# Optimization experiments

Measured on AMD Instinct MI355X. Metric: run time of the kernel, lower is better.

The kernel has to match this reference:

```python
import jax, jax.numpy as jnp
import numpy as np

N, E, IN, OUT, MC, H, C, HID = 50000, 800000, 64, 64, 16, 4, 16, 128
NEG = 0.2   # leaky_relu negative slope
EPS = 1e-5  # BatchNorm eps


def _gcn(x, src, dst, norm, W, b):
    # GCNConv: symmetric-normalized aggregation with self-loops already in (src, dst)
    h = x @ W
    return jax.ops.segment_sum(h[src] * norm[:, None], dst, num_segments=N) + b


def _gat(x, src, dst, W, b, a_s, a_d):
    # GATConv, concat=True: h -> [N, H, C]
    h = (x @ W).reshape(N, H, C)
    e = jax.nn.leaky_relu((h * a_s).sum(-1)[src] + (h * a_d).sum(-1)[dst], NEG)  # [E+N, H]
    m = jax.ops.segment_max(e, dst, num_segments=N)
    p = jnp.exp(e - m[dst])
    alpha = p / jax.ops.segment_sum(p, dst, num_segments=N)[dst]
    out = jax.ops.segment_sum(h[src] * alpha[..., None], dst, num_segments=N)
    return out.reshape(N, H * C) + b


def _bn(x):
    # BatchNorm(affine=False), training stats (biased variance)
    mu = x.mean(0)
    var = x.var(0)
    return (x - mu) / jnp.sqrt(var + EPS)


def _spade(x, mask, src, dst, norm, w0, b0, wg, bg, wb, bb):
    mf = jax.nn.relu(_gcn(mask, src, dst, norm, w0, b0))
    gamma = _gcn(mf, src, dst, norm, wg, bg)
    beta = _gcn(mf, src, dst, norm, wb, bb)
    return _bn(x) * (1.0 + gamma) + beta


def _forward(x, mask, edge_index, params):
    s1, s2, sk, g1, g2, gk = params
    loop = jnp.arange(N, dtype=edge_index.dtype)  # self-loops (GCN & GAT defaults)
    src = jnp.concatenate([edge_index[0], loop])
    dst = jnp.concatenate([edge_index[1], loop])
    deg = jax.ops.segment_sum(jnp.ones(src.shape[0], x.dtype), dst, num_segments=N)
    dinv = jnp.where(deg > 0, jax.lax.rsqrt(deg), 0.0)
    norm = dinv[src] * dinv[dst]
    xm = jax.nn.leaky_relu(_spade(x, mask, src, dst, norm, *s1), NEG)
    xm = _gat(xm, src, dst, *g1)
    xm = jax.nn.leaky_relu(_spade(xm, mask, src, dst, norm, *s2), NEG)
    xm = _gat(xm, src, dst, *g2)
    xs = jax.nn.leaky_relu(_spade(x, mask, src, dst, norm, *sk), NEG)
    xs = _gat(xs, src, dst, *gk)
    return xm + xs


def setup_inputs() -> dict:
    key = jax.random.key(0)
    ks = iter(jax.random.split(key, 40))
    def rn(shape, scale=1.0):
        return jax.random.normal(next(ks), shape, jnp.float32) * scale
    inp = {
        "x": rn((N, IN)),
        "mask": rn((N, MC)),
        "edge_index": jax.random.randint(next(ks), (2, E), 0, N, dtype=jnp.int32),
    }
    for p in ("s1", "s2", "sk"):
        inp[p + "_w0"] = rn((MC, HID), 0.1)
        inp[p + "_b0"] = jnp.zeros(HID, jnp.float32)
        inp[p + "_wg"] = rn((HID, IN), 0.05)
        inp[p + "_bg"] = jnp.zeros(IN, jnp.float32)
        inp[p + "_wb"] = rn((HID, IN), 0.05)
        inp[p + "_bb"] = jnp.zeros(IN, jnp.float32)
    for g, din in (("g1", IN), ("g2", OUT), ("gk", IN)):
        inp[g + "_w"] = rn((din, H * C), 0.1)
        inp[g + "_b"] = jnp.zeros(H * C, jnp.float32)
        inp[g + "_as"] = rn((H, C), 0.1)
        inp[g + "_ad"] = rn((H, C), 0.1)
    return inp


def reference(x, mask, edge_index,
              s1_w0, s1_b0, s1_wg, s1_bg, s1_wb, s1_bb,
              s2_w0, s2_b0, s2_wg, s2_bg, s2_wb, s2_bb,
              sk_w0, sk_b0, sk_wg, sk_bg, sk_wb, sk_bb,
              g1_w, g1_b, g1_as, g1_ad,
              g2_w, g2_b, g2_as, g2_ad,
              gk_w, gk_b, gk_as, gk_ad):
    params = (
        (s1_w0, s1_b0, s1_wg, s1_bg, s1_wb, s1_bb),
        (s2_w0, s2_b0, s2_wg, s2_bg, s2_wb, s2_bb),
        (sk_w0, sk_b0, sk_wg, sk_bg, sk_wb, sk_bb),
        (g1_w, g1_b, g1_as, g1_ad),
        (g2_w, g2_b, g2_as, g2_ad),
        (gk_w, gk_b, gk_as, gk_ad),
    )
    return _forward(x, mask, edge_index, params)
```

## Files before the change

### kernel.cpp

```cpp
#include <hip/hip_runtime.h>
#include <hip/hip_bf16.h>

constexpr int kN   = 50000;
constexpr int kE   = 800000;
constexpr int kIN  = 64;
constexpr int kMC  = 16;
constexpr int kH   = 4;
constexpr int kC   = 16;
constexpr int kHID = 128;
constexpr float kNEG = 0.2f;
constexpr float kEPS = 1e-5f;

__device__ __forceinline__ float lrelu(float x) { return x > 0.f ? x : kNEG * x; }


__global__ void k_count(const int* __restrict__ ei, int* __restrict__ cnt) {
    int e = blockIdx.x * blockDim.x + threadIdx.x;
    if (e < kE) atomicAdd(&cnt[ei[kE + e]], 1);
}

__global__ void k_scan(const int* __restrict__ cnt, int* __restrict__ rp,
                       float* __restrict__ dinv) {
    __shared__ int wsum[16];
    __shared__ int chunk_base;
    int tid = threadIdx.x, lane = tid & 63, wid = tid >> 6;
    if (tid == 0) chunk_base = 0;
    __syncthreads();
    for (int base = 0; base < kN; base += 1024) {
        int i = base + tid;
        int v = (i < kN) ? cnt[i] : 0;
        if (i < kN) dinv[i] = rsqrtf((float)(v + 1));
        int s = v;
        #pragma unroll
        for (int off = 1; off < 64; off <<= 1) {
            int t = __shfl_up(s, off);
            if (lane >= off) s += t;
        }
        if (lane == 63) wsum[wid] = s;
        __syncthreads();
        if (wid == 0) {
            int t = (lane < 16) ? wsum[lane] : 0;
            #pragma unroll
            for (int off = 1; off < 16; off <<= 1) {
                int u = __shfl_up(t, off);
                if (lane >= off) t += u;
            }
            if (lane < 16) wsum[lane] = t;
        }
        __syncthreads();
        int wbase = (wid > 0) ? wsum[wid - 1] : 0;
        int total = wsum[15];
        int excl = chunk_base + wbase + s - v;
        if (i < kN) rp[i] = excl;
        __syncthreads();
        if (tid == 0) chunk_base += total;
        __syncthreads();
    }
    if (threadIdx.x == 0) rp[kN] = chunk_base;
}

__global__ void k_fill(const int* __restrict__ ei, const int* __restrict__ rp,
                       int* __restrict__ fill, int* __restrict__ col) {
    int e = blockIdx.x * blockDim.x + threadIdx.x;
    if (e < kE) {
        int d = ei[kE + e];
        int pos = rp[d] + atomicAdd(&fill[d], 1);
        col[pos] = ei[e];
    }
}


template <int F>
__global__ void k_agg(const float* __restrict__ in, float* __restrict__ out,
                      const float* __restrict__ dinv, const int* __restrict__ rp,
                      const int* __restrict__ col) {
    constexpr int NPB = 256 / F;
    int node = blockIdx.x * NPB + threadIdx.x / F;
    int f = threadIdx.x % F;
    if (node >= kN) return;
    float dv = dinv[node];
    float acc = dv * in[(size_t)node * F + f];
    int b = rp[node], e2 = rp[node + 1];
    for (int i = b; i < e2; ++i) {
        int u = col[i];
        acc += dinv[u] * in[(size_t)u * F + f];
    }
    out[(size_t)node * F + f] = dv * acc;
}


__global__ void k_agg128v(const float* __restrict__ in, float* __restrict__ out,
                          const float* __restrict__ dinv, const int* __restrict__ rp,
                          const int* __restrict__ col) {
    int node = blockIdx.x * 8 + threadIdx.x / 32;
    int l = threadIdx.x & 31;
    if (node >= kN) return;
    const float4* in4 = (const float4*)in;
    float dv = dinv[node];
    float4 acc = in4[(size_t)node * 32 + l];
    int b = rp[node], e2 = rp[node + 1];
    for (int base = b; base < e2; base += 32) {
        int idx = base + l;
        int myu = (idx < e2) ? col[idx] : 0;
        int n = min(32, e2 - base);
        for (int cc = 0; cc < n; ++cc) {
            int u = __shfl(myu, cc, 32);
            float4 w = in4[(size_t)u * 32 + l];
            acc.x += w.x; acc.y += w.y; acc.z += w.z; acc.w += w.w;
        }
    }
    ((float4*)out)[(size_t)node * 32 + l] =
        make_float4(dv * acc.x, dv * acc.y, dv * acc.z, dv * acc.w);
}


__global__ void k_mf(const float* __restrict__ am, const float* __restrict__ w0,
                     const float* __restrict__ b0, const float* __restrict__ dinv,
                     float* __restrict__ mf) {
    __shared__ float w[16 * 128];
    __shared__ float a[16 * 16];
    int tid = threadIdx.x;
    int n0 = blockIdx.x * 16;
    {
        const float4* w04 = (const float4*)w0;
        float4* w4 = (float4*)w;
        #pragma unroll
        for (int i = 0; i < 2; ++i) w4[tid + 256 * i] = w04[tid + 256 * i];
        if (tid < 64) {
            const float4* am4 = (const float4*)am;
            int node = n0 + tid / 4;
            ((float4*)a)[tid] = (node < kN) ? am4[(size_t)node * 4 + (tid & 3)]
                                            : make_float4(0.f, 0.f, 0.f, 0.f);
        }
    }
    __syncthreads();
    int f = tid % 128, g = tid / 128;
    float bf = b0[f];
    for (int j = 0; j < 8; ++j) {
        int nl = g * 8 + j;
        int node = n0 + nl;
        if (node < kN) {
            float acc = bf;
            #pragma unroll
            for (int k = 0; k < 16; ++k) acc += a[nl * 16 + k] * w[k * 128 + f];
            mf[(size_t)node * 128 + f] = dinv[node] * fmaxf(acc, 0.f);
        }
    }
}


__global__ void k_bnstats(const float* __restrict__ x, float* __restrict__ stats) {
    int f = threadIdx.x % 64, r0 = threadIdx.x / 64;
    float s = 0.f, s2 = 0.f;
    for (int v = blockIdx.x * 4 + r0; v < kN; v += gridDim.x * 4) {
        float val = x[(size_t)v * 64 + f];
        s += val; s2 += val * val;
    }
    __shared__ float sh[256], sh2[256];
    sh[threadIdx.x] = s; sh2[threadIdx.x] = s2;
    __syncthreads();
    if (threadIdx.x < 64) {
        s  = sh[threadIdx.x]  + sh[threadIdx.x + 64]  + sh[threadIdx.x + 128]  + sh[threadIdx.x + 192];
        s2 = sh2[threadIdx.x] + sh2[threadIdx.x + 64] + sh2[threadIdx.x + 128] + sh2[threadIdx.x + 192];
        atomicAdd(&stats[f], s);
        atomicAdd(&stats[64 + f], s2);
    }
}

__global__ void k_bnfin(const float* __restrict__ stats, float* __restrict__ mu_rstd) {
    int f = threadIdx.x;
    if (f < 64) {
        float mu = stats[f] / (float)kN;
        float var = stats[64 + f] / (float)kN - mu * mu;
        mu_rstd[f] = mu;
        mu_rstd[64 + f] = rsqrtf(var + kEPS);
    }
}


__global__ void k_spgat(const float* __restrict__ xin, const float* __restrict__ amf,
                        const float* __restrict__ wg, const float* __restrict__ bg,
                        const float* __restrict__ wb, const float* __restrict__ bb,
                        const float* __restrict__ mu_rstd,
                        const float* __restrict__ W, const float* __restrict__ as_,
                        const float* __restrict__ ad_,
                        float* __restrict__ h, float* __restrict__ esed) {
    __shared__ float smem[6144];
    float* a   = smem;
    float* wgs = smem + 2048;
    float* wbs = smem + 4096;
    float* ys  = smem;
    float* ws  = smem + 1024;
    int tid = threadIdx.x;
    int n0 = blockIdx.x * 16;
    {
        const float4* amf4 = (const float4*)amf;
        float4* a4 = (float4*)a;
        #pragma unroll
        for (int i = 0; i < 2; ++i) {
            int idx = tid + 256 * i;
            int node = n0 + idx / 32;
            a4[idx] = (node < kN) ? amf4[(size_t)node * 32 + (idx & 31)]
                                  : make_float4(0.f, 0.f, 0.f, 0.f);
        }
    }
    int f = tid % 64, nl = tid / 64;
    float accg[4] = {0, 0, 0, 0}, accb[4] = {0, 0, 0, 0};
    const float4* wg4 = (const float4*)wg;
    const float4* wb4 = (const float4*)wb;
    for (int c = 0; c < 4; ++c) {
        __syncthreads();
        {
            float4* wgs4 = (float4*)wgs;
            float4* wbs4 = (float4*)wbs;
            #pragma unroll
            for (int i = 0; i < 2; ++i) {
                int idx = tid + 256 * i;
                wgs4[idx] = wg4[c * 512 + idx];
                wbs4[idx] = wb4[c * 512 + idx];
            }
        }
        __syncthreads();
        #pragma unroll
        for (int kk = 0; kk < 32; ++kk) {
            float wgk = wgs[kk * 64 + f], wbk = wbs[kk * 64 + f];
            int k = c * 32 + kk;
            #pragma unroll
            for (int j = 0; j < 4; ++j) {
                float av = a[(j * 4 + nl) * 128 + k];
                accg[j] += av * wgk;
                accb[j] += av * wbk;
            }
        }
    }
    float mu = mu_rstd[f], rstd = mu_rstd[64 + f];
    float bgf = bg[f], bbf = bb[f];
    float yv[4];
    #pragma unroll
    for (int j = 0; j < 4; ++j) {
        int node = n0 + j * 4 + nl;
        if (node < kN) {
            float xv = xin[(size_t)node * 64 + f];
            float g = accg[j] + bgf, b = accb[j] + bbf;
            yv[j] = lrelu((xv - mu) * rstd * (1.f + g) + b);
        } else yv[j] = 0.f;
    }
    __syncthreads();
    #pragma unroll
    for (int j = 0; j < 4; ++j) ys[(j * 4 + nl) * 64 + f] = yv[j];
    {
        const float4* W4 = (const float4*)W;
        float4* ws4 = (float4*)ws;
        #pragma unroll
        for (int i = 0; i < 4; ++i) ws4[tid + 256 * i] = W4[tid + 256 * i];
    }
    __syncthreads();
    float asf = as_[f], adf = ad_[f];
    float acc[4] = {0, 0, 0, 0};
    for (int k = 0; k < 64; ++k) {
        float w = ws[k * 64 + f];
        #pragma unroll
        for (int j = 0; j < 4; ++j) acc[j] += ys[(j * 4 + nl) * 64 + k] * w;
    }
    #pragma unroll
    for (int j = 0; j < 4; ++j) {
        int node = n0 + j * 4 + nl;
        float hv = acc[j];
        float es = hv * asf, ed = hv * adf;
        #pragma unroll
        for (int off = 1; off < 16; off <<= 1) {
            es += __shfl_xor(es, off);
            ed += __shfl_xor(ed, off);
        }
        if (node < kN) {
            h[(size_t)node * 64 + f] = hv;
            if ((f & 15) == 0) {
                int hh = f >> 4;
                esed[node * 8 + hh] = es;
                esed[node * 8 + 4 + hh] = ed;
            }
        }
    }
}


__global__ void k_gatagg(const float* __restrict__ h, const float* __restrict__ esed,
                         const int* __restrict__ rp, const int* __restrict__ col,
                         const float* __restrict__ bias, float* __restrict__ out) {
    int node = blockIdx.x * 4 + threadIdx.x / 64;
    if (node >= kN) return;
    int lane = threadIdx.x & 63;
    int hh = lane >> 4;
    float edv = esed[node * 8 + 4 + hh];
    float m = lrelu(esed[node * 8 + hh] + edv);
    float d = 1.f;
    float acc = h[(size_t)node * 64 + lane];
    int b = rp[node], e2 = rp[node + 1];
    for (int base = b; base < e2; base += 64) {
        int idx = base + lane;
        int myu = (idx < e2) ? col[idx] : 0;
        int n = min(64, e2 - base);
        for (int cc = 0; cc < n; ++cc) {
            int u = __shfl(myu, cc);
            float e = lrelu(esed[u * 8 + hh] + edv);
            float hu = h[(size_t)u * 64 + lane];
            if (e <= m) {
                float p = __expf(e - m);
                d += p;
                acc += p * hu;
            } else {
                float s = __expf(m - e);
                d = d * s + 1.f;
                acc = acc * s + hu;
                m = e;
            }
        }
    }
    out[(size_t)node * 64 + lane] = acc / d + bias[lane];
}


__global__ void k_add(const float4* __restrict__ a, const float4* __restrict__ b,
                      float4* __restrict__ o, int n4) {
    int i = blockIdx.x * blockDim.x + threadIdx.x;
    if (i < n4) {
        float4 x = a[i], y = b[i];
        o[i] = make_float4(x.x + y.x, x.y + y.y, x.z + y.z, x.w + y.w);
    }
}


extern "C" void kernel_launch(void* const* d_in, const int* in_sizes, int n_in,
                              void* d_out, int out_size, void* d_ws, size_t ws_size,
                              hipStream_t stream) {
    const float* x    = (const float*)d_in[0];
    const float* mask = (const float*)d_in[1];
    const int*   ei   = (const int*)d_in[2];
    const float* s_w0[3] = {(const float*)d_in[3],  (const float*)d_in[9],  (const float*)d_in[15]};
    const float* s_b0[3] = {(const float*)d_in[4],  (const float*)d_in[10], (const float*)d_in[16]};
    const float* s_wg[3] = {(const float*)d_in[5],  (const float*)d_in[11], (const float*)d_in[17]};
    const float* s_bg[3] = {(const float*)d_in[6],  (const float*)d_in[12], (const float*)d_in[18]};
    const float* s_wb[3] = {(const float*)d_in[7],  (const float*)d_in[13], (const float*)d_in[19]};
    const float* s_bb[3] = {(const float*)d_in[8],  (const float*)d_in[14], (const float*)d_in[20]};
    const float* g_w[3]  = {(const float*)d_in[21], (const float*)d_in[25], (const float*)d_in[29]};
    const float* g_b[3]  = {(const float*)d_in[22], (const float*)d_in[26], (const float*)d_in[30]};
    const float* g_as[3] = {(const float*)d_in[23], (const float*)d_in[27], (const float*)d_in[31]};
    const float* g_ad[3] = {(const float*)d_in[24], (const float*)d_in[28], (const float*)d_in[32]};

    char* base = (char*)d_ws;
    size_t off = 0;
    auto alloc = [&](size_t bytes) -> void* {
        void* p = base + off;
        off = (off + bytes + 255) & ~(size_t)255;
        return p;
    };
    int*   cnt   = (int*)alloc((size_t)kN * 4);
    int*   rp    = (int*)alloc((size_t)(kN + 1) * 4);
    int*   fill  = (int*)alloc((size_t)kN * 4);
    int*   col   = (int*)alloc((size_t)kE * 4);
    float* dinv  = (float*)alloc((size_t)kN * 4);
    float* am    = (float*)alloc((size_t)kN * 16 * 4);
    float* P     = (float*)alloc((size_t)kN * 128 * 4);
    float* Q     = (float*)alloc((size_t)kN * 128 * 4);
    float* tH    = (float*)alloc((size_t)kN * 64 * 4);
    float* tZ    = (float*)alloc((size_t)kN * 64 * 4);
    float* tZ2   = (float*)alloc((size_t)kN * 64 * 4);
    float* esed  = (float*)alloc((size_t)kN * 8 * 4);
    float* sraw  = (float*)alloc(128 * 4);
    float* st_x  = (float*)alloc(128 * 4);
    float* st_z  = (float*)alloc(128 * 4);
    (void)ws_size; (void)n_in; (void)in_sizes; (void)out_size;

    const int EB = (kE + 255) / 256;

    hipMemsetAsync(cnt, 0, (size_t)kN * 4, stream);
    hipMemsetAsync(fill, 0, (size_t)kN * 4, stream);
    k_count<<<EB, 256, 0, stream>>>(ei, cnt);
    k_scan<<<1, 1024, 0, stream>>>(cnt, rp, dinv);
    k_fill<<<EB, 256, 0, stream>>>(ei, rp, fill, col);

    k_agg<16><<<(kN + 15) / 16, 256, 0, stream>>>(mask, am, dinv, rp, col);
    hipMemsetAsync(sraw, 0, 128 * 4, stream);
    k_bnstats<<<256, 256, 0, stream>>>(x, sraw);
    k_bnfin<<<1, 64, 0, stream>>>(sraw, st_x);

    const int GB16 = (kN + 15) / 16;
    const int GB8  = (kN + 7) / 8;
    const int GB4  = (kN + 3) / 4;

    k_mf<<<GB16, 256, 0, stream>>>(am, s_w0[0], s_b0[0], dinv, P);
    k_agg128v<<<GB8, 256, 0, stream>>>(P, Q, dinv, rp, col);
    k_spgat<<<GB16, 256, 0, stream>>>(x, Q, s_wg[0], s_bg[0], s_wb[0], s_bb[0], st_x,
                                      g_w[0], g_as[0], g_ad[0], tH, esed);
    k_gatagg<<<GB4, 256, 0, stream>>>(tH, esed, rp, col, g_b[0], tZ);

    hipMemsetAsync(sraw, 0, 128 * 4, stream);
    k_bnstats<<<256, 256, 0, stream>>>(tZ, sraw);
    k_bnfin<<<1, 64, 0, stream>>>(sraw, st_z);
    k_mf<<<GB16, 256, 0, stream>>>(am, s_w0[1], s_b0[1], dinv, P);
    k_agg128v<<<GB8, 256, 0, stream>>>(P, Q, dinv, rp, col);
    k_spgat<<<GB16, 256, 0, stream>>>(tZ, Q, s_wg[1], s_bg[1], s_wb[1], s_bb[1], st_z,
                                      g_w[1], g_as[1], g_ad[1], tH, esed);
    k_gatagg<<<GB4, 256, 0, stream>>>(tH, esed, rp, col, g_b[1], tZ2);

    k_mf<<<GB16, 256, 0, stream>>>(am, s_w0[2], s_b0[2], dinv, P);
    k_agg128v<<<GB8, 256, 0, stream>>>(P, Q, dinv, rp, col);
    k_spgat<<<GB16, 256, 0, stream>>>(x, Q, s_wg[2], s_bg[2], s_wb[2], s_bb[2], st_x,
                                      g_w[2], g_as[2], g_ad[2], tH, esed);
    k_gatagg<<<GB4, 256, 0, stream>>>(tH, esed, rp, col, g_b[2], tZ);

    k_add<<<(kN * 64 / 4 + 255) / 256, 256, 0, stream>>>((const float4*)tZ2, (const float4*)tZ,
                                                         (float4*)d_out, kN * 64 / 4);
}
```

Baseline: 1.489 ms.

## Store intermediates in fp16, batch independent branches, fuse GAT aggregations and BN prep

Intermediate mask-feature buffers and GAT hidden features are now stored as fp16, cutting gather bandwidth in the edge aggregations. The skip branch (sk/gk) is batched with the second main-path layer in shared launches, and the two final GAT aggregations are fused with the output add. BN stats finalisation is folded into the spgat kernel, the mask aggregation is merged with the x BN stats into one launch, and the memsets are consolidated. Bounds checks are removed on the assumption that N divides by 16. Half precision lowers accuracy.

```diff
diff --git a/kernel.cpp b/kernel.cpp
--- a/kernel.cpp
+++ b/kernel.cpp
@@ -1,17 +1,19 @@
 #include <hip/hip_runtime.h>
-#include <hip/hip_bf16.h>
+#include <hip/hip_fp16.h>
 
 constexpr int kN   = 50000;
 constexpr int kE   = 800000;
-constexpr int kIN  = 64;
-constexpr int kMC  = 16;
-constexpr int kH   = 4;
-constexpr int kC   = 16;
-constexpr int kHID = 128;
 constexpr float kNEG = 0.2f;
 constexpr float kEPS = 1e-5f;
+constexpr int kNB16 = kN / 16;
 
 __device__ __forceinline__ float lrelu(float x) { return x > 0.f ? x : kNEG * x; }
+
+__device__ __forceinline__ void unpack8(int4 raw, float* t) {
+    __half2* h = (__half2*)&raw;
+    #pragma unroll
+    for (int i = 0; i < 4; ++i) { float2 f = __half22float2(h[i]); t[2*i] = f.x; t[2*i+1] = f.y; }
+}
 
 
 __global__ void k_count(const int* __restrict__ ei, int* __restrict__ cnt) {
@@ -70,80 +72,37 @@
 }
 
 
-template <int F>
-__global__ void k_agg(const float* __restrict__ in, float* __restrict__ out,
-                      const float* __restrict__ dinv, const int* __restrict__ rp,
-                      const int* __restrict__ col) {
-    constexpr int NPB = 256 / F;
-    int node = blockIdx.x * NPB + threadIdx.x / F;
-    int f = threadIdx.x % F;
-    if (node >= kN) return;
-    float dv = dinv[node];
-    float acc = dv * in[(size_t)node * F + f];
-    int b = rp[node], e2 = rp[node + 1];
-    for (int i = b; i < e2; ++i) {
-        int u = col[i];
-        acc += dinv[u] * in[(size_t)u * F + f];
-    }
-    out[(size_t)node * F + f] = dv * acc;
-}
-
-
-__global__ void k_agg128v(const float* __restrict__ in, float* __restrict__ out,
-                          const float* __restrict__ dinv, const int* __restrict__ rp,
-                          const int* __restrict__ col) {
-    int node = blockIdx.x * 8 + threadIdx.x / 32;
-    int l = threadIdx.x & 31;
-    if (node >= kN) return;
-    const float4* in4 = (const float4*)in;
-    float dv = dinv[node];
-    float4 acc = in4[(size_t)node * 32 + l];
-    int b = rp[node], e2 = rp[node + 1];
-    for (int base = b; base < e2; base += 32) {
-        int idx = base + l;
-        int myu = (idx < e2) ? col[idx] : 0;
-        int n = min(32, e2 - base);
-        for (int cc = 0; cc < n; ++cc) {
-            int u = __shfl(myu, cc, 32);
-            float4 w = in4[(size_t)u * 32 + l];
-            acc.x += w.x; acc.y += w.y; acc.z += w.z; acc.w += w.w;
-        }
-    }
-    ((float4*)out)[(size_t)node * 32 + l] =
-        make_float4(dv * acc.x, dv * acc.y, dv * acc.z, dv * acc.w);
-}
-
-
-__global__ void k_mf(const float* __restrict__ am, const float* __restrict__ w0,
-                     const float* __restrict__ b0, const float* __restrict__ dinv,
-                     float* __restrict__ mf) {
-    __shared__ float w[16 * 128];
-    __shared__ float a[16 * 16];
-    int tid = threadIdx.x;
-    int n0 = blockIdx.x * 16;
-    {
-        const float4* w04 = (const float4*)w0;
-        float4* w4 = (float4*)w;
-        #pragma unroll
-        for (int i = 0; i < 2; ++i) w4[tid + 256 * i] = w04[tid + 256 * i];
-        if (tid < 64) {
-            const float4* am4 = (const float4*)am;
-            int node = n0 + tid / 4;
-            ((float4*)a)[tid] = (node < kN) ? am4[(size_t)node * 4 + (tid & 3)]
-                                            : make_float4(0.f, 0.f, 0.f, 0.f);
-        }
-    }
-    __syncthreads();
-    int f = tid % 128, g = tid / 128;
-    float bf = b0[f];
-    for (int j = 0; j < 8; ++j) {
-        int nl = g * 8 + j;
-        int node = n0 + nl;
-        if (node < kN) {
-            float acc = bf;
-            #pragma unroll
-            for (int k = 0; k < 16; ++k) acc += a[nl * 16 + k] * w[k * 128 + f];
-            mf[(size_t)node * 128 + f] = dinv[node] * fmaxf(acc, 0.f);
+__global__ void k_combo(const float* __restrict__ mask, const float* __restrict__ x,
+                        const float* __restrict__ dinv, const int* __restrict__ rp,
+                        const int* __restrict__ col,
+                        float* __restrict__ am, float* __restrict__ sraw_x) {
+    if (blockIdx.x < kNB16) {
+        int node = blockIdx.x * 16 + threadIdx.x / 16;
+        int f = threadIdx.x % 16;
+        float dv = dinv[node];
+        float acc = dv * mask[(size_t)node * 16 + f];
+        int b = rp[node], e2 = rp[node + 1];
+        for (int i = b; i < e2; ++i) {
+            int u = col[i];
+            acc += dinv[u] * mask[(size_t)u * 16 + f];
+        }
+        am[(size_t)node * 16 + f] = dv * acc;
+    } else {
+        int bb = blockIdx.x - kNB16;
+        int f = threadIdx.x % 64, r0 = threadIdx.x / 64;
+        float s = 0.f, s2 = 0.f;
+        for (int v = bb * 4 + r0; v < kN; v += 256 * 4) {
+            float val = x[(size_t)v * 64 + f];
+            s += val; s2 += val * val;
+        }
+        __shared__ float sh[256], sh2[256];
+        sh[threadIdx.x] = s; sh2[threadIdx.x] = s2;
+        __syncthreads();
+        if (threadIdx.x < 64) {
+            s  = sh[threadIdx.x]  + sh[threadIdx.x + 64]  + sh[threadIdx.x + 128]  + sh[threadIdx.x + 192];
+            s2 = sh2[threadIdx.x] + sh2[threadIdx.x + 64] + sh2[threadIdx.x + 128] + sh2[threadIdx.x + 192];
+            atomicAdd(&sraw_x[f], s);
+            atomicAdd(&sraw_x[64 + f], s2);
         }
     }
 }
@@ -167,24 +126,89 @@
     }
 }
 
-__global__ void k_bnfin(const float* __restrict__ stats, float* __restrict__ mu_rstd) {
-    int f = threadIdx.x;
-    if (f < 64) {
-        float mu = stats[f] / (float)kN;
-        float var = stats[64 + f] / (float)kN - mu * mu;
-        mu_rstd[f] = mu;
-        mu_rstd[64 + f] = rsqrtf(var + kEPS);
-    }
-}
-
-
-__global__ void k_spgat(const float* __restrict__ xin, const float* __restrict__ amf,
-                        const float* __restrict__ wg, const float* __restrict__ bg,
-                        const float* __restrict__ wb, const float* __restrict__ bb,
-                        const float* __restrict__ mu_rstd,
-                        const float* __restrict__ W, const float* __restrict__ as_,
-                        const float* __restrict__ ad_,
-                        float* __restrict__ h, float* __restrict__ esed) {
+
+__global__ void k_mf2(const float* __restrict__ am,
+                      const float* __restrict__ w0a, const float* __restrict__ b0a,
+                      const float* __restrict__ w0b, const float* __restrict__ b0b,
+                      const float* __restrict__ dinv,
+                      __half* __restrict__ Pa, __half* __restrict__ Pb) {
+    int set = blockIdx.x / kNB16;
+    int blk = blockIdx.x - set * kNB16;
+    const float* w0 = set ? w0b : w0a;
+    const float* b0 = set ? b0b : b0a;
+    __half* P = set ? Pb : Pa;
+    __shared__ float w[16 * 128];
+    __shared__ float a[16 * 16];
+    int tid = threadIdx.x;
+    int n0 = blk * 16;
+    {
+        const float4* w04 = (const float4*)w0;
+        float4* w4 = (float4*)w;
+        #pragma unroll
+        for (int i = 0; i < 2; ++i) w4[tid + 256 * i] = w04[tid + 256 * i];
+        if (tid < 64) {
+            const float4* am4 = (const float4*)am;
+            int node = n0 + tid / 4;
+            ((float4*)a)[tid] = am4[(size_t)node * 4 + (tid & 3)];
+        }
+    }
+    __syncthreads();
+    int f = tid % 128, g = tid / 128;
+    float bf = b0[f];
+    for (int j = 0; j < 8; ++j) {
+        int nl = g * 8 + j;
+        int node = n0 + nl;
+        float acc = bf;
+        #pragma unroll
+        for (int k = 0; k < 16; ++k) acc += a[nl * 16 + k] * w[k * 128 + f];
+        P[(size_t)node * 128 + f] = __float2half(dinv[node] * fmaxf(acc, 0.f));
+    }
+}
+
+
+__global__ void k_aggh(const __half* __restrict__ Pa, const __half* __restrict__ Pb,
+                       __half* __restrict__ Qa, __half* __restrict__ Qb,
+                       const float* __restrict__ dinv, const int* __restrict__ rp,
+                       const int* __restrict__ col) {
+    int set = blockIdx.x / kNB16;
+    int blk = blockIdx.x - set * kNB16;
+    const int4* in = (const int4*)(set ? Pb : Pa);
+    int4* out = (int4*)(set ? Qb : Qa);
+    int node = blk * 16 + threadIdx.x / 16;
+    int l = threadIdx.x & 15;
+    float dv = dinv[node];
+    float acc[8];
+    unpack8(in[(size_t)node * 16 + l], acc);
+    int b = rp[node], e2 = rp[node + 1];
+    for (int base = b; base < e2; base += 16) {
+        int idx = base + l;
+        int myu = (idx < e2) ? col[idx] : 0;
+        int n = min(16, e2 - base);
+        for (int cc = 0; cc < n; ++cc) {
+            int u = __shfl(myu, cc, 16);
+            float t[8];
+            unpack8(in[(size_t)u * 16 + l], t);
+            #pragma unroll
+            for (int q = 0; q < 8; ++q) acc[q] += t[q];
+        }
+    }
+    int4 r;
+    __half2* hp = (__half2*)&r;
+    #pragma unroll
+    for (int i = 0; i < 4; ++i) hp[i] = __floats2half2_rn(dv * acc[2*i], dv * acc[2*i+1]);
+    out[(size_t)node * 16 + l] = r;
+}
+
+
+struct SpgatArgs {
+    const float* xin; const __half* Q;
+    const float *wg, *bg, *wb, *bb, *sraw, *W, *as_, *ad_;
+    __half* h; float* esed; int eslot;
+};
+
+__global__ void k_spgat(SpgatArgs A, SpgatArgs B) {
+    SpgatArgs P = (blockIdx.x < kNB16) ? A : B;
+    int blk = (blockIdx.x < kNB16) ? blockIdx.x : blockIdx.x - kNB16;
     __shared__ float smem[6144];
     float* a   = smem;
     float* wgs = smem + 2048;
@@ -192,22 +216,20 @@
     float* ys  = smem;
     float* ws  = smem + 1024;
     int tid = threadIdx.x;
-    int n0 = blockIdx.x * 16;
-    {
-        const float4* amf4 = (const float4*)amf;
-        float4* a4 = (float4*)a;
-        #pragma unroll
-        for (int i = 0; i < 2; ++i) {
-            int idx = tid + 256 * i;
-            int node = n0 + idx / 32;
-            a4[idx] = (node < kN) ? amf4[(size_t)node * 32 + (idx & 31)]
-                                  : make_float4(0.f, 0.f, 0.f, 0.f);
-        }
+    int n0 = blk * 16;
+    {
+        const int4* q4 = (const int4*)P.Q;
+        int node = n0 + tid / 16, h8 = tid & 15;
+        float t[8];
+        unpack8(q4[(size_t)node * 16 + h8], t);
+        float* dst = a + (tid / 16) * 128 + h8 * 8;
+        ((float4*)dst)[0] = make_float4(t[0], t[1], t[2], t[3]);
+        ((float4*)dst)[1] = make_float4(t[4], t[5], t[6], t[7]);
     }
     int f = tid % 64, nl = tid / 64;
-    float accg[4] = {0, 0, 0, 0}, accb[4] = {0, 0, 0, 0};
-    const float4* wg4 = (const float4*)wg;
-    const float4* wb4 = (const float4*)wb;
+    float accg[4] = {0,0,0,0}, accb[4] = {0,0,0,0};
+    const float4* wg4 = (const float4*)P.wg;
+    const float4* wb4 = (const float4*)P.wb;
     for (int c = 0; c < 4; ++c) {
         __syncthreads();
         {
@@ -233,30 +255,33 @@
             }
         }
     }
-    float mu = mu_rstd[f], rstd = mu_rstd[64 + f];
-    float bgf = bg[f], bbf = bb[f];
+    float mu, rstd;
+    {
+        float s = P.sraw[f], s2 = P.sraw[64 + f];
+        mu = s * (1.f / kN);
+        rstd = rsqrtf(s2 * (1.f / kN) - mu * mu + kEPS);
+    }
+    float bgf = P.bg[f], bbf = P.bb[f];
     float yv[4];
     #pragma unroll
     for (int j = 0; j < 4; ++j) {
         int node = n0 + j * 4 + nl;
-        if (node < kN) {
-            float xv = xin[(size_t)node * 64 + f];
-            float g = accg[j] + bgf, b = accb[j] + bbf;
-            yv[j] = lrelu((xv - mu) * rstd * (1.f + g) + b);
-        } else yv[j] = 0.f;
+        float xv = P.xin[(size_t)node * 64 + f];
+        float g = accg[j] + bgf, b = accb[j] + bbf;
+        yv[j] = lrelu((xv - mu) * rstd * (1.f + g) + b);
     }
     __syncthreads();
     #pragma unroll
     for (int j = 0; j < 4; ++j) ys[(j * 4 + nl) * 64 + f] = yv[j];
     {
-        const float4* W4 = (const float4*)W;
+        const float4* W4 = (const float4*)P.W;
         float4* ws4 = (float4*)ws;
         #pragma unroll
         for (int i = 0; i < 4; ++i) ws4[tid + 256 * i] = W4[tid + 256 * i];
     }
     __syncthreads();
-    float asf = as_[f], adf = ad_[f];
-    float acc[4] = {0, 0, 0, 0};
+    float asf = P.as_[f], adf = P.ad_[f];
+    float acc[4] = {0,0,0,0};
     for (int k = 0; k < 64; ++k) {
         float w = ws[k * 64 + f];
         #pragma unroll
@@ -272,29 +297,26 @@
             es += __shfl_xor(es, off);
             ed += __shfl_xor(ed, off);
         }
-        if (node < kN) {
-            h[(size_t)node * 64 + f] = hv;
-            if ((f & 15) == 0) {
-                int hh = f >> 4;
-                esed[node * 8 + hh] = es;
-                esed[node * 8 + 4 + hh] = ed;
-            }
-        }
-    }
-}
-
-
-__global__ void k_gatagg(const float* __restrict__ h, const float* __restrict__ esed,
-                         const int* __restrict__ rp, const int* __restrict__ col,
-                         const float* __restrict__ bias, float* __restrict__ out) {
+        P.h[(size_t)node * 64 + f] = __float2half(hv);
+        if ((f & 15) == 0) {
+            int hh = f >> 4;
+            P.esed[node * 16 + P.eslot + hh] = es;
+            P.esed[node * 16 + P.eslot + 4 + hh] = ed;
+        }
+    }
+}
+
+
+__global__ void k_gatagg1(const __half* __restrict__ h, const float* __restrict__ esed,
+                          const int* __restrict__ rp, const int* __restrict__ col,
+                          const float* __restrict__ bias, float* __restrict__ out) {
     int node = blockIdx.x * 4 + threadIdx.x / 64;
-    if (node >= kN) return;
     int lane = threadIdx.x & 63;
     int hh = lane >> 4;
-    float edv = esed[node * 8 + 4 + hh];
-    float m = lrelu(esed[node * 8 + hh] + edv);
+    float edv = esed[node * 16 + 4 + hh];
+    float m = lrelu(esed[node * 16 + hh] + edv);
     float d = 1.f;
-    float acc = h[(size_t)node * 64 + lane];
+    float acc = __half2float(h[(size_t)node * 64 + lane]);
     int b = rp[node], e2 = rp[node + 1];
     for (int base = b; base < e2; base += 64) {
         int idx = base + lane;
@@ -302,17 +324,14 @@
         int n = min(64, e2 - base);
         for (int cc = 0; cc < n; ++cc) {
             int u = __shfl(myu, cc);
-            float e = lrelu(esed[u * 8 + hh] + edv);
-            float hu = h[(size_t)u * 64 + lane];
+            float e = lrelu(esed[u * 16 + hh] + edv);
+            float hu = __half2float(h[(size_t)u * 64 + lane]);
             if (e <= m) {
                 float p = __expf(e - m);
-                d += p;
-                acc += p * hu;
+                d += p; acc += p * hu;
             } else {
                 float s = __expf(m - e);
-                d = d * s + 1.f;
-                acc = acc * s + hu;
-                m = e;
+                d = d * s + 1.f; acc = acc * s + hu; m = e;
             }
         }
     }
@@ -320,13 +339,39 @@
 }
 
 
-__global__ void k_add(const float4* __restrict__ a, const float4* __restrict__ b,
-                      float4* __restrict__ o, int n4) {
-    int i = blockIdx.x * blockDim.x + threadIdx.x;
-    if (i < n4) {
-        float4 x = a[i], y = b[i];
-        o[i] = make_float4(x.x + y.x, x.y + y.y, x.z + y.z, x.w + y.w);
-    }
+__global__ void k_gatagg2(const __half* __restrict__ h2, const __half* __restrict__ hk,
+                          const float* __restrict__ esed,
+                          const int* __restrict__ rp, const int* __restrict__ col,
+                          const float* __restrict__ b2, const float* __restrict__ bk,
+                          float* __restrict__ out) {
+    int node = blockIdx.x * 4 + threadIdx.x / 64;
+    int lane = threadIdx.x & 63;
+    int hh = lane >> 4;
+    float ed2 = esed[node * 16 + 4 + hh];
+    float edk = esed[node * 16 + 12 + hh];
+    float m2 = lrelu(esed[node * 16 + hh] + ed2);
+    float mk = lrelu(esed[node * 16 + 8 + hh] + edk);
+    float d2 = 1.f, dk = 1.f;
+    float a2 = __half2float(h2[(size_t)node * 64 + lane]);
+    float ak = __half2float(hk[(size_t)node * 64 + lane]);
+    int b = rp[node], e2 = rp[node + 1];
+    for (int base = b; base < e2; base += 64) {
+        int idx = base + lane;
+        int myu = (idx < e2) ? col[idx] : 0;
+        int n = min(64, e2 - base);
+        for (int cc = 0; cc < n; ++cc) {
+            int u = __shfl(myu, cc);
+            float q2 = lrelu(esed[u * 16 + hh] + ed2);
+            float qk = lrelu(esed[u * 16 + 8 + hh] + edk);
+            float h2u = __half2float(h2[(size_t)u * 64 + lane]);
+            float hku = __half2float(hk[(size_t)u * 64 + lane]);
+            if (q2 <= m2) { float p = __expf(q2 - m2); d2 += p; a2 += p * h2u; }
+            else { float s = __expf(m2 - q2); d2 = d2 * s + 1.f; a2 = a2 * s + h2u; m2 = q2; }
+            if (qk <= mk) { float p = __expf(qk - mk); dk += p; ak += p * hku; }
+            else { float s = __expf(mk - qk); dk = dk * s + 1.f; ak = ak * s + hku; mk = qk; }
+        }
+    }
+    out[(size_t)node * 64 + lane] = a2 / d2 + b2[lane] + ak / dk + bk[lane];
 }
 
 
@@ -354,61 +399,52 @@
         off = (off + bytes + 255) & ~(size_t)255;
         return p;
     };
-    int*   cnt   = (int*)alloc((size_t)kN * 4);
-    int*   rp    = (int*)alloc((size_t)(kN + 1) * 4);
-    int*   fill  = (int*)alloc((size_t)kN * 4);
-    int*   col   = (int*)alloc((size_t)kE * 4);
-    float* dinv  = (float*)alloc((size_t)kN * 4);
-    float* am    = (float*)alloc((size_t)kN * 16 * 4);
-    float* P     = (float*)alloc((size_t)kN * 128 * 4);
-    float* Q     = (float*)alloc((size_t)kN * 128 * 4);
-    float* tH    = (float*)alloc((size_t)kN * 64 * 4);
-    float* tZ    = (float*)alloc((size_t)kN * 64 * 4);
-    float* tZ2   = (float*)alloc((size_t)kN * 64 * 4);
-    float* esed  = (float*)alloc((size_t)kN * 8 * 4);
-    float* sraw  = (float*)alloc(128 * 4);
-    float* st_x  = (float*)alloc(128 * 4);
-    float* st_z  = (float*)alloc(128 * 4);
+    int*   cnt    = (int*)alloc((size_t)kN * 4);
+    int*   fill   = (int*)alloc((size_t)kN * 4);
+    float* sraw_x = (float*)alloc(128 * 4);
+    float* sraw_z = (float*)alloc(128 * 4);
+    size_t zero_span = off;
+    int*    rp    = (int*)alloc((size_t)(kN + 1) * 4);
+    int*    col   = (int*)alloc((size_t)kE * 4);
+    float*  dinv  = (float*)alloc((size_t)kN * 4);
+    float*  am    = (float*)alloc((size_t)kN * 16 * 4);
+    __half* Pa    = (__half*)alloc((size_t)kN * 128 * 2);
+    __half* Pb    = (__half*)alloc((size_t)kN * 128 * 2);
+    __half* Qa    = (__half*)alloc((size_t)kN * 128 * 2);
+    __half* Qb    = (__half*)alloc((size_t)kN * 128 * 2);
+    __half* hA    = (__half*)alloc((size_t)kN * 64 * 2);
+    __half* hB    = (__half*)alloc((size_t)kN * 64 * 2);
+    float*  esed  = (float*)alloc((size_t)kN * 16 * 4);
+    float*  z1    = (float*)alloc((size_t)kN * 64 * 4);
     (void)ws_size; (void)n_in; (void)in_sizes; (void)out_size;
 
     const int EB = (kE + 255) / 256;
-
-    hipMemsetAsync(cnt, 0, (size_t)kN * 4, stream);
-    hipMemsetAsync(fill, 0, (size_t)kN * 4, stream);
+    const int GB4 = kN / 4;
+
+    hipMemsetAsync(cnt, 0, zero_span, stream);
     k_count<<<EB, 256, 0, stream>>>(ei, cnt);
     k_scan<<<1, 1024, 0, stream>>>(cnt, rp, dinv);
     k_fill<<<EB, 256, 0, stream>>>(ei, rp, fill, col);
-
-    k_agg<16><<<(kN + 15) / 16, 256, 0, stream>>>(mask, am, dinv, rp, col);
-    hipMemsetAsync(sraw, 0, 128 * 4, stream);
-    k_bnstats<<<256, 256, 0, stream>>>(x, sraw);
-    k_bnfin<<<1, 64, 0, stream>>>(sraw, st_x);
-
-    const int GB16 = (kN + 15) / 16;
-    const int GB8  = (kN + 7) / 8;
-    const int GB4  = (kN + 3) / 4;
-
-    k_mf<<<GB16, 256, 0, stream>>>(am, s_w0[0], s_b0[0], dinv, P);
-    k_agg128v<<<GB8, 256, 0, stream>>>(P, Q, dinv, rp, col);
-    k_spgat<<<GB16, 256, 0, stream>>>(x, Q, s_wg[0], s_bg[0], s_wb[0], s_bb[0], st_x,
-                                      g_w[0], g_as[0], g_ad[0], tH, esed);
-    k_gatagg<<<GB4, 256, 0, stream>>>(tH, esed, rp, col, g_b[0], tZ);
-
-    hipMemsetAsync(sraw, 0, 128 * 4, stream);
-    k_bnstats<<<256, 256, 0, stream>>>(tZ, sraw);
-    k_bnfin<<<1, 64, 0, stream>>>(sraw, st_z);
-    k_mf<<<GB16, 256, 0, stream>>>(am, s_w0[1], s_b0[1], dinv, P);
-    k_agg128v<<<GB8, 256, 0, stream>>>(P, Q, dinv, rp, col);
-    k_spgat<<<GB16, 256, 0, stream>>>(tZ, Q, s_wg[1], s_bg[1], s_wb[1], s_bb[1], st_z,
-                                      g_w[1], g_as[1], g_ad[1], tH, esed);
-    k_gatagg<<<GB4, 256, 0, stream>>>(tH, esed, rp, col, g_b[1], tZ2);
-
-    k_mf<<<GB16, 256, 0, stream>>>(am, s_w0[2], s_b0[2], dinv, P);
-    k_agg128v<<<GB8, 256, 0, stream>>>(P, Q, dinv, rp, col);
-    k_spgat<<<GB16, 256, 0, stream>>>(x, Q, s_wg[2], s_bg[2], s_wb[2], s_bb[2], st_x,
-                                      g_w[2], g_as[2], g_ad[2], tH, esed);
-    k_gatagg<<<GB4, 256, 0, stream>>>(tH, esed, rp, col, g_b[2], tZ);
-
-    k_add<<<(kN * 64 / 4 + 255) / 256, 256, 0, stream>>>((const float4*)tZ2, (const float4*)tZ,
-                                                         (float4*)d_out, kN * 64 / 4);
-}
+    k_combo<<<kNB16 + 256, 256, 0, stream>>>(mask, x, dinv, rp, col, am, sraw_x);
+
+    k_mf2<<<kNB16, 256, 0, stream>>>(am, s_w0[0], s_b0[0], s_w0[0], s_b0[0], dinv, Pa, Pb);
+    k_aggh<<<kNB16, 256, 0, stream>>>(Pa, Pb, Qa, Qb, dinv, rp, col);
+    {
+        SpgatArgs A{x, Qa, s_wg[0], s_bg[0], s_wb[0], s_bb[0], sraw_x,
+                    g_w[0], g_as[0], g_ad[0], hA, esed, 0};
+        k_spgat<<<kNB16, 256, 0, stream>>>(A, A);
+    }
+    k_gatagg1<<<GB4, 256, 0, stream>>>(hA, esed, rp, col, g_b[0], z1);
+
+    k_bnstats<<<256, 256, 0, stream>>>(z1, sraw_z);
+    k_mf2<<<2 * kNB16, 256, 0, stream>>>(am, s_w0[1], s_b0[1], s_w0[2], s_b0[2], dinv, Pa, Pb);
+    k_aggh<<<2 * kNB16, 256, 0, stream>>>(Pa, Pb, Qa, Qb, dinv, rp, col);
+    {
+        SpgatArgs A{z1, Qa, s_wg[1], s_bg[1], s_wb[1], s_bb[1], sraw_z,
+                    g_w[1], g_as[1], g_ad[1], hA, esed, 0};
+        SpgatArgs B{x,  Qb, s_wg[2], s_bg[2], s_wb[2], s_bb[2], sraw_x,
+                    g_w[2], g_as[2], g_ad[2], hB, esed, 8};
+        k_spgat<<<2 * kNB16, 256, 0, stream>>>(A, B);
+    }
+    k_gatagg2<<<GB4, 256, 0, stream>>>(hA, hB, esed, rp, col, g_b[1], g_b[2], (float*)d_out);
+}
```

New measurement: 1.240 ms. 16.7% less time.
